# Kernel optimization log

Measured on AMD Instinct MI355X. Metric: run time of the kernel, lower is better.

Reference implementation:

```python
import math
import jax, jax.numpy as jnp
import numpy as np

B, S, H = 8, 2048, 1024
NH = 1
DH = H // NH          # head dim == hidden since NH=1 (required by module's math)
DT = 64               # distance_type


def setup_inputs() -> dict:
    key = jax.random.key(0)
    ks = jax.random.split(key, 10)
    hidden_states = jax.random.normal(ks[0], (B, S, H), dtype=jnp.float32)
    attention_mask = jnp.zeros((B, 1, 1, S), dtype=jnp.float32)
    word_word_relation = jax.random.randint(ks[1], (B, S, S), 0, DT, dtype=jnp.int32)
    init = 0.02
    Wq = jax.random.normal(ks[2], (H, H), dtype=jnp.float32) * init
    bq = jnp.zeros((H,), dtype=jnp.float32)
    Wk = jax.random.normal(ks[3], (H, H), dtype=jnp.float32) * init
    bk = jnp.zeros((H,), dtype=jnp.float32)
    Wv = jax.random.normal(ks[4], (H, H), dtype=jnp.float32) * init
    bv = jnp.zeros((H,), dtype=jnp.float32)
    dist_emb = jax.random.normal(ks[5], (DT, H), dtype=jnp.float32) * init
    dist_emb = dist_emb.at[0].set(0.0)  # padding_idx=0
    return {
        "hidden_states": hidden_states,
        "attention_mask": attention_mask,
        "word_word_relation": word_word_relation,
        "Wq": Wq, "bq": bq, "Wk": Wk, "bk": bk, "Wv": Wv, "bv": bv,
        "dist_emb": dist_emb,
    }


def reference(hidden_states, attention_mask, word_word_relation,
              Wq, bq, Wk, bk, Wv, bv, dist_emb):
    b, s, h = hidden_states.shape
    def heads(x):  # [b,s,h] -> [b,nh,s,dh]
        return x.reshape(b, s, NH, DH).transpose(0, 2, 1, 3)
    q = heads(hidden_states @ Wq.T + bq)
    k = heads(hidden_states @ Wk.T + bk)
    v = heads(hidden_states @ Wv.T + bv)

    scores = jnp.einsum('bhqd,bhkd->bhqk', q, k)                 # [b,nh,s,s]
    word_dot_distance = jnp.einsum('bhqd,td->bhqt', q, dist_emb) # [b,nh,s,DT]

    idx = word_word_relation[:, None, :, :]                      # [b,1,s,s]
    bias = jnp.take_along_axis(word_dot_distance, idx, axis=3)
    mask_out = (word_word_relation == 1)[:, None].astype(scores.dtype)
    bias = bias * mask_out

    scores = (scores + bias) / math.sqrt(DH) + attention_mask
    probs = jax.nn.softmax(scores, axis=-1)
    ctx = jnp.einsum('bhqk,bhkd->bhqd', probs, v)
    ctx = ctx.transpose(0, 2, 1, 3).reshape(b, s, h)
    return ctx
```

## Files before the change

kernel.cpp:

```cpp
#include <hip/hip_runtime.h>

typedef unsigned short u16;
typedef __bf16 bf16x8 __attribute__((ext_vector_type(8)));
typedef float f32x4 __attribute__((ext_vector_type(4)));

#define S_LEN 2048
#define H_LEN 1024

__device__ __forceinline__ u16 f2b(float f) {
  unsigned u = __float_as_uint(f);
  return (u16)((u + 0x7FFFu + ((u >> 16) & 1u)) >> 16);
}
__device__ __forceinline__ float b2f(u16 h) { return __uint_as_float(((unsigned)h) << 16); }

#define GLOAD16(gp, lp)                                   \
  __builtin_amdgcn_global_load_lds(                       \
      (__attribute__((address_space(1))) void*)(gp),      \
      (__attribute__((address_space(3))) void*)(lp), 16, 0, 0)

__global__ __launch_bounds__(256) void prep_kernel(
    const float* __restrict__ X, const float* __restrict__ Wq,
    const float* __restrict__ Wk, const float* __restrict__ Wv,
    const float* __restrict__ bq, const float* __restrict__ bk,
    const float* __restrict__ bv, const float* __restrict__ dist,
    u16* __restrict__ Xbf, u16* __restrict__ Wbf, float* __restrict__ b_all,
    u16* __restrict__ de1, float* __restrict__ lsum) {
  size_t tid = (size_t)blockIdx.x * blockDim.x + threadIdx.x;
  size_t nth = (size_t)gridDim.x * blockDim.x;
  for (size_t i = tid; i < 4194304u; i += nth) {
    float4 v = ((const float4*)X)[i];
    ushort4 o; o.x = f2b(v.x); o.y = f2b(v.y); o.z = f2b(v.z); o.w = f2b(v.w);
    ((ushort4*)Xbf)[i] = o;
  }
  for (size_t i = tid; i < 786432u; i += nth) {
    int which = (int)(i >> 18);
    size_t off = i & 262143u;
    const float4* src = (const float4*)(which == 0 ? Wq : (which == 1 ? Wk : Wv));
    float4 v = src[off];
    ushort4 o; o.x = f2b(v.x); o.y = f2b(v.y); o.z = f2b(v.z); o.w = f2b(v.w);
    ((ushort4*)Wbf)[i] = o;
  }
  for (size_t i = tid; i < 256u; i += nth) {
    float4 v = ((const float4*)(dist + H_LEN))[i];
    ushort4 o; o.x = f2b(v.x); o.y = f2b(v.y); o.z = f2b(v.z); o.w = f2b(v.w);
    ((ushort4*)de1)[i] = o;
  }
  for (size_t i = tid; i < 3072u; i += nth)
    b_all[i] = (i < 1024) ? bq[i] : (i < 2048 ? bk[i - 1024] : bv[i - 2048]);
  for (size_t i = tid; i < 16384u; i += nth) lsum[i] = 0.f;
}

struct GArgs {
  const u16* A; const u16* B;
  long long sA, sB;
  int ldA, ldB, K;
  u16 *Qo, *Ko, *Vo; const float* b_all;
  const int* rel; const float* d1; const float* mask; u16* P; float* lsum;
  const float* lin; float* outp;
};

template <int EPI>
__global__ __launch_bounds__(256) void gemm_nt(GArgs g) {
  const int bz = blockIdx.z;
  const u16* Abase = g.A + (size_t)bz * g.sA;
  const u16* Bbase = g.B + (size_t)bz * g.sB;
  const int m0 = blockIdx.y * 128, n0 = blockIdx.x * 128;
  __shared__ u16 As[128 * 32];
  __shared__ u16 Bs[128 * 32];
  const int tid = threadIdx.x;
  const int lane = tid & 63, w = tid >> 6;
  const int wm = w >> 1, wn = w & 1;
  const int l15 = lane & 15, quad = lane >> 4;

  f32x4 acc[4][4];
  const f32x4 zero = {0.f, 0.f, 0.f, 0.f};
#pragma unroll
  for (int a = 0; a < 4; ++a)
#pragma unroll
    for (int b = 0; b < 4; ++b) acc[a][b] = zero;

  const int c0 = tid, c1 = tid + 256;
  const u16* ga0 = Abase + (size_t)(m0 + (c0 >> 2)) * g.ldA + (c0 & 3) * 8;
  const u16* ga1 = Abase + (size_t)(m0 + (c1 >> 2)) * g.ldA + (c1 & 3) * 8;
  const u16* gb0 = Bbase + (size_t)(n0 + (c0 >> 2)) * g.ldB + (c0 & 3) * 8;
  const u16* gb1 = Bbase + (size_t)(n0 + (c1 >> 2)) * g.ldB + (c1 & 3) * 8;
  u16* la0 = &As[c0 * 8]; u16* la1 = &As[c1 * 8];
  u16* lb0 = &Bs[c0 * 8]; u16* lb1 = &Bs[c1 * 8];

  for (int kt = 0; kt < g.K; kt += 32) {
    __syncthreads();
    GLOAD16(ga0 + kt, la0);
    GLOAD16(ga1 + kt, la1);
    GLOAD16(gb0 + kt, lb0);
    GLOAD16(gb1 + kt, lb1);
    __syncthreads();
    bf16x8 af[4], bfb[4];
#pragma unroll
    for (int t = 0; t < 4; ++t) {
      af[t]  = *(const bf16x8*)&As[(wm * 64 + t * 16 + l15) * 32 + quad * 8];
      bfb[t] = *(const bf16x8*)&Bs[(wn * 64 + t * 16 + l15) * 32 + quad * 8];
    }
#pragma unroll
    for (int mt = 0; mt < 4; ++mt)
#pragma unroll
      for (int nt = 0; nt < 4; ++nt)
        acc[mt][nt] = __builtin_amdgcn_mfma_f32_16x16x32_bf16(af[mt], bfb[nt], acc[mt][nt], 0, 0, 0);
  }

  if constexpr (EPI == 0) {
#pragma unroll
    for (int mt = 0; mt < 4; ++mt)
#pragma unroll
      for (int r = 0; r < 4; ++r) {
        const int i = m0 + wm * 64 + mt * 16 + quad * 4 + r;
#pragma unroll
        for (int nt = 0; nt < 4; ++nt) {
          const int n = n0 + wn * 64 + nt * 16 + l15;
          const float v = acc[mt][nt][r] + g.b_all[n];
          const int which = n >> 10, nl = n & 1023;
          u16* dst = which == 0 ? g.Qo : (which == 1 ? g.Ko : g.Vo);
          dst[(size_t)i * H_LEN + nl] = f2b(v);
        }
      }
  }
  if constexpr (EPI == 1) {
    const size_t bSS = (size_t)bz * S_LEN * S_LEN;
#pragma unroll
    for (int mt = 0; mt < 4; ++mt) {
#pragma unroll
      for (int r = 0; r < 4; ++r) {
        const int i = m0 + wm * 64 + mt * 16 + quad * 4 + r;
        const float d1v = g.d1[bz * S_LEN + i];
        const size_t rowo = bSS + (size_t)i * S_LEN;
        float psum = 0.f;
#pragma unroll
        for (int nt = 0; nt < 4; ++nt) {
          const int j = n0 + wn * 64 + nt * 16 + l15;
          const int rv = g.rel[rowo + j];
          const float logit = (acc[mt][nt][r] + (rv == 1 ? d1v : 0.f)) * 0.03125f
                              + g.mask[bz * S_LEN + j];
          const float p = __expf(logit);
          g.P[rowo + j] = f2b(p);
          psum += p;
        }
        psum += __shfl_xor(psum, 1);
        psum += __shfl_xor(psum, 2);
        psum += __shfl_xor(psum, 4);
        psum += __shfl_xor(psum, 8);
        if (l15 == 0) atomicAdd(&g.lsum[bz * S_LEN + i], psum);
      }
    }
  }
  if constexpr (EPI == 2) {
    const size_t ob = (size_t)bz * S_LEN * H_LEN;
#pragma unroll
    for (int mt = 0; mt < 4; ++mt)
#pragma unroll
      for (int r = 0; r < 4; ++r) {
        const int i = m0 + wm * 64 + mt * 16 + quad * 4 + r;
        const float inv = 1.0f / g.lin[bz * S_LEN + i];
        const size_t rowo = ob + (size_t)i * H_LEN;
#pragma unroll
        for (int nt = 0; nt < 4; ++nt) {
          const int d = n0 + wn * 64 + nt * 16 + l15;
          g.outp[rowo + d] = acc[mt][nt][r] * inv;
        }
      }
  }
}

__global__ __launch_bounds__(256) void compute_d1(const u16* __restrict__ Q,
                                                  const u16* __restrict__ de1,
                                                  float* __restrict__ d1) {
  const int gid = blockIdx.x * 256 + threadIdx.x;
  const int row = gid >> 6, lane = gid & 63;
  const u16* q = Q + ((size_t)row << 10);
  float s = 0.f;
#pragma unroll
  for (int it = 0; it < 2; ++it) {
    const int k0 = it * 512 + lane * 8;
    ushort4 qa = *(const ushort4*)(q + k0);
    ushort4 qb = *(const ushort4*)(q + k0 + 4);
    ushort4 da = *(const ushort4*)(de1 + k0);
    ushort4 db = *(const ushort4*)(de1 + k0 + 4);
    s += b2f(qa.x) * b2f(da.x) + b2f(qa.y) * b2f(da.y) +
         b2f(qa.z) * b2f(da.z) + b2f(qa.w) * b2f(da.w) +
         b2f(qb.x) * b2f(db.x) + b2f(qb.y) * b2f(db.y) +
         b2f(qb.z) * b2f(db.z) + b2f(qb.w) * b2f(db.w);
  }
#pragma unroll
  for (int off = 32; off > 0; off >>= 1) s += __shfl_down(s, off);
  if (lane == 0) d1[row] = s;
}

__global__ __launch_bounds__(256) void transpose_v(const u16* __restrict__ V,
                                                   u16* __restrict__ Vt) {
  const int b = blockIdx.z;
  const int j0 = blockIdx.x * 64;
  const int d0 = blockIdx.y * 64;
  __shared__ u16 t[64][72];
  const int tid = threadIdx.x;
  const int tr = tid >> 4;
  const int tc = (tid & 15) * 4;
#pragma unroll
  for (int p = 0; p < 4; ++p) {
    const int jl = p * 16 + tr;
    const u16* src = V + ((size_t)b * S_LEN + (j0 + jl)) * H_LEN + d0 + tc;
    ushort4 v = *(const ushort4*)src;
    t[jl][tc + 0] = v.x; t[jl][tc + 1] = v.y; t[jl][tc + 2] = v.z; t[jl][tc + 3] = v.w;
  }
  __syncthreads();
#pragma unroll
  for (int p = 0; p < 4; ++p) {
    const int dl = p * 16 + tr;
    ushort4 v;
    v.x = t[tc + 0][dl]; v.y = t[tc + 1][dl]; v.z = t[tc + 2][dl]; v.w = t[tc + 3][dl];
    *(ushort4*)(Vt + ((size_t)b * H_LEN + (d0 + dl)) * S_LEN + j0 + tc) = v;
  }
}

extern "C" void kernel_launch(void* const* d_in, const int* in_sizes, int n_in,
                              void* d_out, int out_size, void* d_ws, size_t ws_size,
                              hipStream_t stream) {
  (void)in_sizes; (void)n_in; (void)out_size; (void)ws_size;
  const float* X    = (const float*)d_in[0];
  const float* mask = (const float*)d_in[1];
  const int*   rel  = (const int*)d_in[2];
  const float* Wq   = (const float*)d_in[3];
  const float* bq   = (const float*)d_in[4];
  const float* Wk   = (const float*)d_in[5];
  const float* bk   = (const float*)d_in[6];
  const float* Wv   = (const float*)d_in[7];
  const float* bv   = (const float*)d_in[8];
  const float* dist = (const float*)d_in[9];
  float* out = (float*)d_out;

  char* p = (char*)d_ws;
  u16* Xbf = (u16*)p;      p += (size_t)16384 * 1024 * 2;
  u16* Wbf = (u16*)p;      p += (size_t)3072 * 1024 * 2;
  float* b_all = (float*)p; p += 3072 * 4;
  u16* de1 = (u16*)p;      p += 4096;
  u16* Qb = (u16*)p;       p += (size_t)16384 * 1024 * 2;
  u16* Kb = (u16*)p;       p += (size_t)16384 * 1024 * 2;
  u16* Vb = (u16*)p;       p += (size_t)16384 * 1024 * 2;
  u16* Vt = (u16*)p;       p += (size_t)16384 * 1024 * 2;
  float* d1 = (float*)p;   p += 16384 * 4;
  float* lsum = (float*)p; p += 16384 * 4;
  u16* P = (u16*)p;        p += (size_t)8 * 2048 * 2048 * 2;

  prep_kernel<<<1024, 256, 0, stream>>>(X, Wq, Wk, Wv, bq, bk, bv, dist,
                                        Xbf, Wbf, b_all, de1, lsum);

  GArgs g0 = {};
  g0.A = Xbf; g0.B = Wbf; g0.sA = 0; g0.sB = 0;
  g0.ldA = 1024; g0.ldB = 1024; g0.K = 1024;
  g0.Qo = Qb; g0.Ko = Kb; g0.Vo = Vb; g0.b_all = b_all;
  gemm_nt<0><<<dim3(24, 128, 1), dim3(256, 1, 1), 0, stream>>>(g0);

  compute_d1<<<4096, 256, 0, stream>>>(Qb, de1, d1);
  transpose_v<<<dim3(32, 16, 8), dim3(256, 1, 1), 0, stream>>>(Vb, Vt);

  GArgs g1 = {};
  g1.A = Qb; g1.B = Kb; g1.sA = 2048LL * 1024; g1.sB = 2048LL * 1024;
  g1.ldA = 1024; g1.ldB = 1024; g1.K = 1024;
  g1.rel = rel; g1.d1 = d1; g1.mask = mask; g1.P = P; g1.lsum = lsum;
  gemm_nt<1><<<dim3(16, 16, 8), dim3(256, 1, 1), 0, stream>>>(g1);

  GArgs g2 = {};
  g2.A = P; g2.B = Vt; g2.sA = 2048LL * 2048; g2.sB = 1024LL * 2048;
  g2.ldA = 2048; g2.ldB = 2048; g2.K = 2048;
  g2.lin = lsum; g2.outp = out;
  gemm_nt<2><<<dim3(8, 16, 8), dim3(256, 1, 1), 0, stream>>>(g2);
}
```

Measured before the change: 686.7 us.

## Fuse d1 into QKV GEMM, pack relation mask to bits, stage epilogues via LDS

Computes the q·dist_emb[1] dot product inside the QKV GEMM epilogue with atomics, which removes the separate compute_d1 kernel. The relation==1 mask is packed into a bitmask by a new pre-pass so the score epilogue reads far fewer bytes. The GEMM K-step grows to 64 and adds a grouped block swizzle for the QKV GEMM. The Q/K/V and P epilogues now write through swizzled shared memory for coalesced 16-byte stores. This adds an extra kernel pass over rel, reuses the Xbf buffer for the bitmask, and d1 now comes from fp32 accumulators before bf16 rounding.

```diff
diff --git a/kernel.cpp b/kernel.cpp
--- a/kernel.cpp
+++ b/kernel.cpp
@@ -2,6 +2,7 @@
 
 typedef unsigned short u16;
 typedef __bf16 bf16x8 __attribute__((ext_vector_type(8)));
+typedef u16 u16x8 __attribute__((ext_vector_type(8)));
 typedef float f32x4 __attribute__((ext_vector_type(4)));
 
 #define S_LEN 2048
@@ -24,7 +25,7 @@
     const float* __restrict__ bq, const float* __restrict__ bk,
     const float* __restrict__ bv, const float* __restrict__ dist,
     u16* __restrict__ Xbf, u16* __restrict__ Wbf, float* __restrict__ b_all,
-    u16* __restrict__ de1, float* __restrict__ lsum) {
+    u16* __restrict__ de1, float* __restrict__ lsum, float* __restrict__ d1) {
   size_t tid = (size_t)blockIdx.x * blockDim.x + threadIdx.x;
   size_t nth = (size_t)gridDim.x * blockDim.x;
   for (size_t i = tid; i < 4194304u; i += nth) {
@@ -47,26 +48,56 @@
   }
   for (size_t i = tid; i < 3072u; i += nth)
     b_all[i] = (i < 1024) ? bq[i] : (i < 2048 ? bk[i - 1024] : bv[i - 2048]);
-  for (size_t i = tid; i < 16384u; i += nth) lsum[i] = 0.f;
+  for (size_t i = tid; i < 16384u; i += nth) { lsum[i] = 0.f; d1[i] = 0.f; }
+}
+
+__global__ __launch_bounds__(256) void relprep_kernel(const int* __restrict__ rel,
+                                                      unsigned* __restrict__ bits) {
+  size_t tid = (size_t)blockIdx.x * blockDim.x + threadIdx.x;
+  size_t nth = (size_t)gridDim.x * blockDim.x;
+  const int4* r4 = (const int4*)rel;
+  for (size_t wi = tid; wi < 1048576u; wi += nth) {
+    const int4* s = r4 + wi * 8;
+    unsigned m = 0;
+#pragma unroll
+    for (int u = 0; u < 8; ++u) {
+      int4 v = s[u];
+      m |= (unsigned)(v.x == 1) << (u * 4 + 0);
+      m |= (unsigned)(v.y == 1) << (u * 4 + 1);
+      m |= (unsigned)(v.z == 1) << (u * 4 + 2);
+      m |= (unsigned)(v.w == 1) << (u * 4 + 3);
+    }
+    bits[wi] = m;
+  }
 }
 
 struct GArgs {
   const u16* A; const u16* B;
   long long sA, sB;
   int ldA, ldB, K;
-  u16 *Qo, *Ko, *Vo; const float* b_all;
-  const int* rel; const float* d1; const float* mask; u16* P; float* lsum;
+  u16 *Qo, *Ko, *Vo; const float* b_all; const u16* de1; float* d1;
+  const unsigned* relbits; const float* mask; u16* P; float* lsum;
   const float* lin; float* outp;
 };
 
 template <int EPI>
 __global__ __launch_bounds__(256) void gemm_nt(GArgs g) {
   const int bz = blockIdx.z;
+  int bx = blockIdx.x, by = blockIdx.y;
+  if constexpr (EPI == 0) {
+    const int lin = by * 24 + bx;
+    const int band = lin / (24 * 8), rem = lin % (24 * 8);
+    by = band * 8 + (rem & 7);
+    bx = rem >> 3;
+  }
   const u16* Abase = g.A + (size_t)bz * g.sA;
   const u16* Bbase = g.B + (size_t)bz * g.sB;
-  const int m0 = blockIdx.y * 128, n0 = blockIdx.x * 128;
-  __shared__ u16 As[128 * 32];
-  __shared__ u16 Bs[128 * 32];
+  const int m0 = by * 128, n0 = bx * 128;
+
+  __shared__ u16 smem[16384];
+  u16* As = smem;
+  u16* Bs = smem + 8192;
+
   const int tid = threadIdx.x;
   const int lane = tid & 63, w = tid >> 6;
   const int wm = w >> 1, wn = w & 1;
@@ -84,73 +115,122 @@
   const u16* ga1 = Abase + (size_t)(m0 + (c1 >> 2)) * g.ldA + (c1 & 3) * 8;
   const u16* gb0 = Bbase + (size_t)(n0 + (c0 >> 2)) * g.ldB + (c0 & 3) * 8;
   const u16* gb1 = Bbase + (size_t)(n0 + (c1 >> 2)) * g.ldB + (c1 & 3) * 8;
-  u16* la0 = &As[c0 * 8]; u16* la1 = &As[c1 * 8];
-  u16* lb0 = &Bs[c0 * 8]; u16* lb1 = &Bs[c1 * 8];
-
-  for (int kt = 0; kt < g.K; kt += 32) {
+  u16* la0 = As + c0 * 8; u16* la1 = As + c1 * 8;
+  u16* lb0 = Bs + c0 * 8; u16* lb1 = Bs + c1 * 8;
+
+  for (int kt = 0; kt < g.K; kt += 64) {
     __syncthreads();
-    GLOAD16(ga0 + kt, la0);
-    GLOAD16(ga1 + kt, la1);
-    GLOAD16(gb0 + kt, lb0);
-    GLOAD16(gb1 + kt, lb1);
+    GLOAD16(ga0 + kt, la0);      GLOAD16(ga0 + kt + 32, la0 + 4096);
+    GLOAD16(ga1 + kt, la1);      GLOAD16(ga1 + kt + 32, la1 + 4096);
+    GLOAD16(gb0 + kt, lb0);      GLOAD16(gb0 + kt + 32, lb0 + 4096);
+    GLOAD16(gb1 + kt, lb1);      GLOAD16(gb1 + kt + 32, lb1 + 4096);
     __syncthreads();
-    bf16x8 af[4], bfb[4];
-#pragma unroll
-    for (int t = 0; t < 4; ++t) {
-      af[t]  = *(const bf16x8*)&As[(wm * 64 + t * 16 + l15) * 32 + quad * 8];
-      bfb[t] = *(const bf16x8*)&Bs[(wn * 64 + t * 16 + l15) * 32 + quad * 8];
+#pragma unroll
+    for (int s = 0; s < 2; ++s) {
+      bf16x8 af[4], bfb[4];
+#pragma unroll
+      for (int t = 0; t < 4; ++t) {
+        af[t]  = *(const bf16x8*)&As[s * 4096 + (wm * 64 + t * 16 + l15) * 32 + quad * 8];
+        bfb[t] = *(const bf16x8*)&Bs[s * 4096 + (wn * 64 + t * 16 + l15) * 32 + quad * 8];
+      }
+#pragma unroll
+      for (int mt = 0; mt < 4; ++mt)
+#pragma unroll
+        for (int nt = 0; nt < 4; ++nt)
+          acc[mt][nt] = __builtin_amdgcn_mfma_f32_16x16x32_bf16(af[mt], bfb[nt], acc[mt][nt], 0, 0, 0);
+    }
+  }
+  __syncthreads();
+
+  const int nbase = n0 + wn * 64;
+
+  if constexpr (EPI == 0) {
+    const int which = n0 >> 10;
+    float bv4[4], dw[4];
+#pragma unroll
+    for (int nt = 0; nt < 4; ++nt) {
+      bv4[nt] = g.b_all[nbase + nt * 16 + l15];
+      dw[nt] = (which == 0) ? b2f(g.de1[nbase + nt * 16 + l15]) : 0.f;
     }
 #pragma unroll
     for (int mt = 0; mt < 4; ++mt)
 #pragma unroll
-      for (int nt = 0; nt < 4; ++nt)
-        acc[mt][nt] = __builtin_amdgcn_mfma_f32_16x16x32_bf16(af[mt], bfb[nt], acc[mt][nt], 0, 0, 0);
-  }
-
-  if constexpr (EPI == 0) {
-#pragma unroll
-    for (int mt = 0; mt < 4; ++mt)
-#pragma unroll
       for (int r = 0; r < 4; ++r) {
-        const int i = m0 + wm * 64 + mt * 16 + quad * 4 + r;
+        const int row = wm * 64 + mt * 16 + quad * 4 + r;
+        float part = 0.f;
 #pragma unroll
         for (int nt = 0; nt < 4; ++nt) {
-          const int n = n0 + wn * 64 + nt * 16 + l15;
-          const float v = acc[mt][nt][r] + g.b_all[n];
-          const int which = n >> 10, nl = n & 1023;
-          u16* dst = which == 0 ? g.Qo : (which == 1 ? g.Ko : g.Vo);
-          dst[(size_t)i * H_LEN + nl] = f2b(v);
+          const float v = acc[mt][nt][r] + bv4[nt];
+          part += v * dw[nt];
+          const int col = wn * 64 + nt * 16 + l15;
+          const int chunkS = (col >> 3) ^ (row & 15);
+          smem[row * 128 + chunkS * 8 + (col & 7)] = f2b(v);
+        }
+        if (which == 0) {
+          part += __shfl_xor(part, 1);
+          part += __shfl_xor(part, 2);
+          part += __shfl_xor(part, 4);
+          part += __shfl_xor(part, 8);
+          if (l15 == 0) atomicAdd(&g.d1[m0 + row], part);
         }
       }
-  }
+    __syncthreads();
+    u16* dstbuf = which == 0 ? g.Qo : (which == 1 ? g.Ko : g.Vo);
+    const int nl0 = n0 & 1023;
+#pragma unroll
+    for (int p = 0; p < 8; ++p) {
+      const int flat = p * 256 + tid;
+      const int row = flat >> 4, chunk = flat & 15;
+      const int chunkS = chunk ^ (row & 15);
+      u16x8 v = *(const u16x8*)&smem[row * 128 + chunkS * 8];
+      *(u16x8*)(dstbuf + (size_t)(m0 + row) * H_LEN + nl0 + chunk * 8) = v;
+    }
+  }
+
   if constexpr (EPI == 1) {
+    float mk[4];
+#pragma unroll
+    for (int nt = 0; nt < 4; ++nt) mk[nt] = g.mask[bz * S_LEN + nbase + nt * 16 + l15];
     const size_t bSS = (size_t)bz * S_LEN * S_LEN;
 #pragma unroll
-    for (int mt = 0; mt < 4; ++mt) {
+    for (int mt = 0; mt < 4; ++mt)
 #pragma unroll
       for (int r = 0; r < 4; ++r) {
-        const int i = m0 + wm * 64 + mt * 16 + quad * 4 + r;
-        const float d1v = g.d1[bz * S_LEN + i];
-        const size_t rowo = bSS + (size_t)i * S_LEN;
+        const int row = wm * 64 + mt * 16 + quad * 4 + r;
+        const int gi = bz * S_LEN + m0 + row;
+        const float d1v = g.d1[gi] * 0.03125f;
+        const unsigned w0 = g.relbits[(size_t)gi * 64 + (nbase >> 5)];
+        const unsigned w1 = g.relbits[(size_t)gi * 64 + (nbase >> 5) + 1];
         float psum = 0.f;
 #pragma unroll
         for (int nt = 0; nt < 4; ++nt) {
-          const int j = n0 + wn * 64 + nt * 16 + l15;
-          const int rv = g.rel[rowo + j];
-          const float logit = (acc[mt][nt][r] + (rv == 1 ? d1v : 0.f)) * 0.03125f
-                              + g.mask[bz * S_LEN + j];
-          const float p = __expf(logit);
-          g.P[rowo + j] = f2b(p);
-          psum += p;
+          const unsigned word = (nt & 2) ? w1 : w0;
+          const int pos = (nt * 16 + l15) & 31;
+          const float bias = ((word >> pos) & 1) ? d1v : 0.f;
+          const float logit = acc[mt][nt][r] * 0.03125f + bias + mk[nt];
+          const float pv = __expf(logit);
+          psum += pv;
+          const int col = wn * 64 + nt * 16 + l15;
+          const int chunkS = (col >> 3) ^ (row & 15);
+          smem[row * 128 + chunkS * 8 + (col & 7)] = f2b(pv);
         }
         psum += __shfl_xor(psum, 1);
         psum += __shfl_xor(psum, 2);
         psum += __shfl_xor(psum, 4);
         psum += __shfl_xor(psum, 8);
-        if (l15 == 0) atomicAdd(&g.lsum[bz * S_LEN + i], psum);
+        if (l15 == 0) atomicAdd(&g.lsum[gi], psum);
       }
-    }
-  }
+    __syncthreads();
+#pragma unroll
+    for (int p = 0; p < 8; ++p) {
+      const int flat = p * 256 + tid;
+      const int row = flat >> 4, chunk = flat & 15;
+      const int chunkS = chunk ^ (row & 15);
+      u16x8 v = *(const u16x8*)&smem[row * 128 + chunkS * 8];
+      *(u16x8*)(g.P + bSS + (size_t)(m0 + row) * S_LEN + n0 + chunk * 8) = v;
+    }
+  }
+
   if constexpr (EPI == 2) {
     const size_t ob = (size_t)bz * S_LEN * H_LEN;
 #pragma unroll
@@ -167,30 +247,6 @@
         }
       }
   }
-}
-
-__global__ __launch_bounds__(256) void compute_d1(const u16* __restrict__ Q,
-                                                  const u16* __restrict__ de1,
-                                                  float* __restrict__ d1) {
-  const int gid = blockIdx.x * 256 + threadIdx.x;
-  const int row = gid >> 6, lane = gid & 63;
-  const u16* q = Q + ((size_t)row << 10);
-  float s = 0.f;
-#pragma unroll
-  for (int it = 0; it < 2; ++it) {
-    const int k0 = it * 512 + lane * 8;
-    ushort4 qa = *(const ushort4*)(q + k0);
-    ushort4 qb = *(const ushort4*)(q + k0 + 4);
-    ushort4 da = *(const ushort4*)(de1 + k0);
-    ushort4 db = *(const ushort4*)(de1 + k0 + 4);
-    s += b2f(qa.x) * b2f(da.x) + b2f(qa.y) * b2f(da.y) +
-         b2f(qa.z) * b2f(da.z) + b2f(qa.w) * b2f(da.w) +
-         b2f(qb.x) * b2f(db.x) + b2f(qb.y) * b2f(db.y) +
-         b2f(qb.z) * b2f(db.z) + b2f(qb.w) * b2f(db.w);
-  }
-#pragma unroll
-  for (int off = 32; off > 0; off >>= 1) s += __shfl_down(s, off);
-  if (lane == 0) d1[row] = s;
 }
 
 __global__ __launch_bounds__(256) void transpose_v(const u16* __restrict__ V,
@@ -247,23 +303,24 @@
   float* d1 = (float*)p;   p += 16384 * 4;
   float* lsum = (float*)p; p += 16384 * 4;
   u16* P = (u16*)p;        p += (size_t)8 * 2048 * 2048 * 2;
+  unsigned* relbits = (unsigned*)Xbf;
 
   prep_kernel<<<1024, 256, 0, stream>>>(X, Wq, Wk, Wv, bq, bk, bv, dist,
-                                        Xbf, Wbf, b_all, de1, lsum);
+                                        Xbf, Wbf, b_all, de1, lsum, d1);
 
   GArgs g0 = {};
   g0.A = Xbf; g0.B = Wbf; g0.sA = 0; g0.sB = 0;
   g0.ldA = 1024; g0.ldB = 1024; g0.K = 1024;
-  g0.Qo = Qb; g0.Ko = Kb; g0.Vo = Vb; g0.b_all = b_all;
+  g0.Qo = Qb; g0.Ko = Kb; g0.Vo = Vb; g0.b_all = b_all; g0.de1 = de1; g0.d1 = d1;
   gemm_nt<0><<<dim3(24, 128, 1), dim3(256, 1, 1), 0, stream>>>(g0);
 
-  compute_d1<<<4096, 256, 0, stream>>>(Qb, de1, d1);
+  relprep_kernel<<<1024, 256, 0, stream>>>(rel, relbits);
   transpose_v<<<dim3(32, 16, 8), dim3(256, 1, 1), 0, stream>>>(Vb, Vt);
 
   GArgs g1 = {};
   g1.A = Qb; g1.B = Kb; g1.sA = 2048LL * 1024; g1.sB = 2048LL * 1024;
   g1.ldA = 1024; g1.ldB = 1024; g1.K = 1024;
-  g1.rel = rel; g1.d1 = d1; g1.mask = mask; g1.P = P; g1.lsum = lsum;
+  g1.relbits = relbits; g1.d1 = d1; g1.mask = mask; g1.P = P; g1.lsum = lsum;
   gemm_nt<1><<<dim3(16, 16, 8), dim3(256, 1, 1), 0, stream>>>(g1);
 
   GArgs g2 = {};
```

After: 684.1 us. No clear change (-0.4%).
